# Kernel optimization log

Measured on AMD Instinct MI355X. Metric: run time of the kernel, lower is better.

Reference implementation:

```python
import jax, jax.numpy as jnp
import numpy as np

BN_EPS = 1e-5


def setup_inputs() -> dict:
    key = jax.random.key(0)
    ks = jax.random.split(key, 13)
    B, C, H, W = 8, 256, 96, 32
    D = C // 2  # inter_channels
    s = 0.05
    return {
        "x": jax.random.normal(ks[0], (B, C, H, W), jnp.float32),
        "g_w": jax.random.normal(ks[1], (D, C), jnp.float32) * s,
        "g_b": jax.random.normal(ks[2], (D,), jnp.float32) * s,
        "theta_w": jax.random.normal(ks[3], (D, C), jnp.float32) * s,
        "theta_b": jax.random.normal(ks[4], (D,), jnp.float32) * s,
        "phi_w": jax.random.normal(ks[5], (D, C), jnp.float32) * s,
        "phi_b": jax.random.normal(ks[6], (D,), jnp.float32) * s,
        "w_w": jax.random.normal(ks[7], (C, D), jnp.float32) * s,
        "w_b": jax.random.normal(ks[8], (C,), jnp.float32) * s,
        "bn_gamma": jax.random.normal(ks[9], (C,), jnp.float32),
        "bn_beta": jax.random.normal(ks[10], (C,), jnp.float32) * s,
        "bn_mean": jax.random.normal(ks[11], (C,), jnp.float32) * s,
        "bn_var": jax.random.uniform(ks[12], (C,), jnp.float32),
    }


def reference(x, g_w, g_b, theta_w, theta_b, phi_w, phi_b, w_w, w_b,
              bn_gamma, bn_beta, bn_mean, bn_var):
    B, C, H, W = x.shape
    N = H * W
    xf = x.reshape(B, C, N)  # flatten spatial: (B, C, N)

    # 1x1 conv projections == per-pixel linear maps
    g_x = jnp.einsum('dc,bcn->bnd', g_w, xf) + g_b            # (B, N, D)
    theta_x = jnp.einsum('dc,bcn->bnd', theta_w, xf) + theta_b  # (B, N, D)
    phi_x = jnp.einsum('dc,bcn->bdn', phi_w, xf) + phi_b[:, None]  # (B, D, N)

    # unnormalized attention: f = theta phi^T / N, then y = f g
    f_div_C = jnp.einsum('bnd,bdm->bnm', theta_x, phi_x) / N  # (B, N, N)
    y = jnp.einsum('bnm,bmd->bnd', f_div_C, g_x)              # (B, N, D)

    # output 1x1 conv + eval-mode BatchNorm2d
    wy = jnp.einsum('cd,bnd->bcn', w_w, y) + w_b[:, None]     # (B, C, N)
    inv = bn_gamma / jnp.sqrt(bn_var + BN_EPS)
    wy = (wy - bn_mean[:, None]) * inv[:, None] + bn_beta[:, None]

    z = wy.reshape(B, C, H, W) + x  # residual
    return z
```

## Files before the change

kernel.cpp:

```cpp
#include <hip/hip_runtime.h>
#include <hip/hip_bf16.h>
#include <cstddef>

typedef __attribute__((ext_vector_type(8))) short short8;
typedef __attribute__((ext_vector_type(4))) float floatx4;
typedef __hip_bfloat16 bf16;

#define NB 8
#define NC 256
#define ND 128
#define NN 3072
#define BN_EPS 1e-5f

static __device__ __forceinline__ short f2s(float v) {
    bf16 h = __float2bfloat16(v);
    return *reinterpret_cast<short*>(&h);
}

__global__ __launch_bounds__(384)
void proj_kernel(const float* __restrict__ x,
                 const float* __restrict__ phi_w, const float* __restrict__ g_w,
                 const float* __restrict__ theta_w,
                 const float* __restrict__ phi_b, const float* __restrict__ g_b,
                 const float* __restrict__ theta_b,
                 short* __restrict__ thND, float* __restrict__ Mbuf)
{
    __shared__ short Ws[384][72];
    __shared__ short Xs[64][72];
    int b = blockIdx.y;
    int n0 = blockIdx.x * 64;
    int t = threadIdx.x;
    int lane = t & 63;
    int wave = t >> 6;
    int lm = lane & 15;
    int lk = (lane >> 4) * 8;

    const float* xb = x + (size_t)b * NC * NN;

    int wk = (t & 7) * 8;
    int wr0 = t >> 3;

    floatx4 zero = {0.f, 0.f, 0.f, 0.f};
    floatx4 acc[4][4];
#pragma unroll
    for (int i = 0; i < 4; ++i)
#pragma unroll
        for (int j = 0; j < 4; ++j) acc[i][j] = zero;

#pragma unroll
    for (int kt = 0; kt < NC; kt += 64) {
        __syncthreads();
#pragma unroll
        for (int p = 0; p < 8; ++p) {
            int r = wr0 + p * 48;
            const float* src = (r < 128) ? (phi_w + (size_t)r * NC)
                             : (r < 256) ? (g_w + (size_t)(r - 128) * NC)
                                         : (theta_w + (size_t)(r - 256) * NC);
            src += kt + wk;
            floatx4 v0 = *(const floatx4*)src;
            floatx4 v1 = *(const floatx4*)(src + 4);
            short8 s;
#pragma unroll
            for (int j = 0; j < 4; ++j) { s[j] = f2s(v0[j]); s[4 + j] = f2s(v1[j]); }
            *(short8*)&Ws[r][wk] = s;
        }
        if (t < 256) {
            int sn = t & 63, cg = t >> 6;
            const float* src = xb + (size_t)(kt + cg * 16) * NN + n0 + sn;
            short8 s0, s1;
#pragma unroll
            for (int j = 0; j < 8; ++j) {
                s0[j] = f2s(src[(size_t)j * NN]);
                s1[j] = f2s(src[(size_t)(8 + j) * NN]);
            }
            *(short8*)&Xs[sn][cg * 16]     = s0;
            *(short8*)&Xs[sn][cg * 16 + 8] = s1;
        }
        __syncthreads();
#pragma unroll
        for (int kk = 0; kk < 64; kk += 32) {
            short8 af[4], bfr[4];
#pragma unroll
            for (int i = 0; i < 4; ++i)
                af[i] = *(const short8*)&Ws[wave * 64 + i * 16 + lm][kk + lk];
#pragma unroll
            for (int j = 0; j < 4; ++j)
                bfr[j] = *(const short8*)&Xs[j * 16 + lm][kk + lk];
#pragma unroll
            for (int i = 0; i < 4; ++i)
#pragma unroll
                for (int j = 0; j < 4; ++j)
                    acc[i][j] = __builtin_amdgcn_mfma_f32_16x16x32_bf16(
                        af[i], bfr[j], acc[i][j], 0, 0, 0);
        }
    }

    int row0 = wave * 64 + (lane >> 4) * 4;

    __syncthreads();
    if (wave < 4) {
#pragma unroll
        for (int i = 0; i < 4; ++i) {
#pragma unroll
            for (int r = 0; r < 4; ++r) {
                int row = row0 + i * 16 + r;
                float bv = (row < 128) ? phi_b[row] : g_b[row - 128];
#pragma unroll
                for (int j = 0; j < 4; ++j)
                    Ws[row][lm + j * 16] = f2s(acc[i][j][r] + bv);
            }
        }
    } else {
        short* Tb = thND + (size_t)b * NN * ND;
#pragma unroll
        for (int i = 0; i < 4; ++i) {
#pragma unroll
            for (int r = 0; r < 4; ++r) {
                int d = row0 - 256 + i * 16 + r;
                float bv = theta_b[d];
#pragma unroll
                for (int j = 0; j < 4; ++j)
                    Tb[(size_t)(n0 + lm + j * 16) * ND + d] =
                        f2s(acc[i][j][r] + bv);
            }
        }
    }
    __syncthreads();

    if (wave < 4) {
        int wr = wave >> 1, wc = wave & 1;
        floatx4 macc[4][4];
#pragma unroll
        for (int i = 0; i < 4; ++i)
#pragma unroll
            for (int j = 0; j < 4; ++j) macc[i][j] = zero;
#pragma unroll
        for (int kk = 0; kk < 64; kk += 32) {
            short8 af[4], bfr[4];
#pragma unroll
            for (int i = 0; i < 4; ++i)
                af[i] = *(const short8*)&Ws[wr * 64 + i * 16 + lm][kk + lk];
#pragma unroll
            for (int j = 0; j < 4; ++j)
                bfr[j] = *(const short8*)&Ws[128 + wc * 64 + j * 16 + lm][kk + lk];
#pragma unroll
            for (int i = 0; i < 4; ++i)
#pragma unroll
                for (int j = 0; j < 4; ++j)
                    macc[i][j] = __builtin_amdgcn_mfma_f32_16x16x32_bf16(
                        af[i], bfr[j], macc[i][j], 0, 0, 0);
        }
        float* Mf = Mbuf + (size_t)b * ND * ND;
        int mr0 = wr * 64 + (lane >> 4) * 4;
        int mc0 = wc * 64 + lm;
        const float sc = 1.f / (float)NN;
#pragma unroll
        for (int i = 0; i < 4; ++i)
#pragma unroll
            for (int j = 0; j < 4; ++j)
#pragma unroll
                for (int r = 0; r < 4; ++r)
                    atomicAdd(&Mf[(size_t)(mr0 + i * 16 + r) * ND + mc0 + j * 16],
                              macc[i][j][r] * sc);
    }
}

__global__ __launch_bounds__(256)
void final_kernel(const float* __restrict__ Mbuf, const short* __restrict__ thND,
                  const float* __restrict__ w_w, const float* __restrict__ w_b,
                  const float* __restrict__ gamma, const float* __restrict__ beta,
                  const float* __restrict__ mean, const float* __restrict__ var,
                  const float* __restrict__ x, float* __restrict__ out)
{
    __shared__ short As[128][72];
    __shared__ short Bs[128][72];
    __shared__ short P2s[128][132];
    int b = blockIdx.z;
    int tile_m = blockIdx.y * 128;
    int tile_n = blockIdx.x * 128;
    int t = threadIdx.x;
    int lane = t & 63;
    int wave = t >> 6;
    int wr = wave >> 1, wc = wave & 1;
    int lm = lane & 15;
    int lk = (lane >> 4) * 8;
    int ch = (t & 7) * 8;
    int r0 = t >> 3;

    const float* Mb = Mbuf + (size_t)b * ND * ND;

    floatx4 zero = {0.f, 0.f, 0.f, 0.f};
    floatx4 acc[4][4];
#pragma unroll
    for (int i = 0; i < 4; ++i)
#pragma unroll
        for (int j = 0; j < 4; ++j) acc[i][j] = zero;

#pragma unroll
    for (int kt = 0; kt < ND; kt += 64) {
        __syncthreads();
#pragma unroll
        for (int p = 0; p < 4; ++p) {
            int r = r0 + p * 32;
            const float* ap = w_w + (size_t)(tile_m + r) * ND + kt + ch;
            const float* bp = Mb + (size_t)r * ND + kt + ch;
            floatx4 a0 = *(const floatx4*)ap, a1 = *(const floatx4*)(ap + 4);
            floatx4 b0 = *(const floatx4*)bp, b1 = *(const floatx4*)(bp + 4);
            short8 sa, sb;
#pragma unroll
            for (int j = 0; j < 4; ++j) {
                sa[j] = f2s(a0[j]); sa[4 + j] = f2s(a1[j]);
                sb[j] = f2s(b0[j]); sb[4 + j] = f2s(b1[j]);
            }
            *(short8*)&As[r][ch] = sa;
            *(short8*)&Bs[r][ch] = sb;
        }
        __syncthreads();
#pragma unroll
        for (int kk = 0; kk < 64; kk += 32) {
            short8 af[4], bfr[4];
#pragma unroll
            for (int i = 0; i < 4; ++i)
                af[i] = *(const short8*)&As[wr * 64 + i * 16 + lm][kk + lk];
#pragma unroll
            for (int j = 0; j < 4; ++j)
                bfr[j] = *(const short8*)&Bs[wc * 64 + j * 16 + lm][kk + lk];
#pragma unroll
            for (int i = 0; i < 4; ++i)
#pragma unroll
                for (int j = 0; j < 4; ++j)
                    acc[i][j] = __builtin_amdgcn_mfma_f32_16x16x32_bf16(
                        af[i], bfr[j], acc[i][j], 0, 0, 0);
        }
    }

    {
        int row0 = wr * 64 + (lane >> 4) * 4;
        int col0 = wc * 64 + lm;
#pragma unroll
        for (int i = 0; i < 4; ++i) {
#pragma unroll
            for (int r = 0; r < 4; ++r) {
                int cl = row0 + i * 16 + r;
                int c = tile_m + cl;
                float iv = gamma[c] * rsqrtf(var[c] + BN_EPS);
#pragma unroll
                for (int j = 0; j < 4; ++j)
                    P2s[cl][col0 + j * 16] = f2s(acc[i][j][r] * iv);
            }
        }
    }
    __syncthreads();

    floatx4 acc2[4][4];
#pragma unroll
    for (int i = 0; i < 4; ++i)
#pragma unroll
        for (int j = 0; j < 4; ++j) acc2[i][j] = zero;

    const short* Tb = thND + (size_t)b * NN * ND;
#pragma unroll
    for (int kt = 0; kt < ND; kt += 64) {
        __syncthreads();
#pragma unroll
        for (int p = 0; p < 4; ++p) {
            int r = r0 + p * 32;
            *(short8*)&Bs[r][ch] =
                *(const short8*)(Tb + (size_t)(tile_n + r) * ND + kt + ch);
        }
        __syncthreads();
#pragma unroll
        for (int kk = 0; kk < 64; kk += 32) {
            short8 af[4], bfr[4];
#pragma unroll
            for (int i = 0; i < 4; ++i)
                af[i] = *(const short8*)&P2s[wr * 64 + i * 16 + lm][kt + kk + lk];
#pragma unroll
            for (int j = 0; j < 4; ++j)
                bfr[j] = *(const short8*)&Bs[wc * 64 + j * 16 + lm][kk + lk];
#pragma unroll
            for (int i = 0; i < 4; ++i)
#pragma unroll
                for (int j = 0; j < 4; ++j)
                    acc2[i][j] = __builtin_amdgcn_mfma_f32_16x16x32_bf16(
                        af[i], bfr[j], acc2[i][j], 0, 0, 0);
        }
    }

    int crow0 = tile_m + wr * 64 + (lane >> 4) * 4;
    int col0 = tile_n + wc * 64 + lm;
    float* Cf = out + (size_t)b * NC * NN;
    const float* Rg = x + (size_t)b * NC * NN;
#pragma unroll
    for (int i = 0; i < 4; ++i) {
#pragma unroll
        for (int r = 0; r < 4; ++r) {
            int c = crow0 + i * 16 + r;
            float iv = gamma[c] * rsqrtf(var[c] + BN_EPS);
            float b2 = iv * (w_b[c] - mean[c]) + beta[c];
#pragma unroll
            for (int j = 0; j < 4; ++j) {
                size_t idx = (size_t)c * NN + col0 + j * 16;
                Cf[idx] = acc2[i][j][r] + b2 + Rg[idx];
            }
        }
    }
}

extern "C" void kernel_launch(void* const* d_in, const int* in_sizes, int n_in,
                              void* d_out, int out_size, void* d_ws, size_t ws_size,
                              hipStream_t stream)
{
    const float* x       = (const float*)d_in[0];
    const float* g_w     = (const float*)d_in[1];
    const float* g_b     = (const float*)d_in[2];
    const float* theta_w = (const float*)d_in[3];
    const float* theta_b = (const float*)d_in[4];
    const float* phi_w   = (const float*)d_in[5];
    const float* phi_b   = (const float*)d_in[6];
    const float* w_w     = (const float*)d_in[7];
    const float* w_b     = (const float*)d_in[8];
    const float* gamma   = (const float*)d_in[9];
    const float* beta    = (const float*)d_in[10];
    const float* mean    = (const float*)d_in[11];
    const float* var     = (const float*)d_in[12];
    (void)in_sizes; (void)n_in; (void)out_size; (void)ws_size;

    char* w = (char*)d_ws;
    short* thND = (short*)w; w += (size_t)NB * NN * ND * 2;
    float* Mbuf = (float*)w; w += (size_t)NB * ND * ND * 4;

    proj_kernel<<<dim3(NN / 64, NB), dim3(384), 0, stream>>>(
        x, phi_w, g_w, theta_w, phi_b, g_b, theta_b, thND, Mbuf);

    final_kernel<<<dim3(NN / 128, NC / 128, NB), 256, 0, stream>>>(
        Mbuf, thND, w_w, w_b, gamma, beta, mean, var, x, (float*)d_out);
}
```

Measured before the change: 161.3 us.

## Pre-convert projection weights to bf16 and store theta transposed

Adds a small setup kernel that converts the phi/g/theta weights to bf16 once per call. The projection kernel then reads A-fragments directly from global memory instead of staging and converting them in shared memory per block. Theta output is stored in D-major layout so its writes are contiguous in N, and the final kernel transposes it into shared memory with scalar scatters. Two redundant barriers are removed. The costs are an extra launch, uncached-in-LDS global fragment loads, and possible LDS bank conflicts in the transpose.

```diff
diff --git a/kernel.cpp b/kernel.cpp
--- a/kernel.cpp
+++ b/kernel.cpp
@@ -17,15 +17,25 @@
     return *reinterpret_cast<short*>(&h);
 }
 
+__global__ __launch_bounds__(256) void setup_kernel(
+    const float* __restrict__ phi_w, const float* __restrict__ g_w,
+    const float* __restrict__ theta_w, short* __restrict__ Wall)
+{
+    int t = threadIdx.x;
+    int r = blockIdx.x;
+    const float* src = (r < 128) ? (phi_w + (size_t)r * NC)
+                     : (r < 256) ? (g_w + (size_t)(r - 128) * NC)
+                                 : (theta_w + (size_t)(r - 256) * NC);
+    Wall[(size_t)r * NC + t] = f2s(src[t]);
+}
+
 __global__ __launch_bounds__(384)
-void proj_kernel(const float* __restrict__ x,
-                 const float* __restrict__ phi_w, const float* __restrict__ g_w,
-                 const float* __restrict__ theta_w,
+void proj_kernel(const float* __restrict__ x, const short* __restrict__ Wall,
                  const float* __restrict__ phi_b, const float* __restrict__ g_b,
                  const float* __restrict__ theta_b,
-                 short* __restrict__ thND, float* __restrict__ Mbuf)
+                 short* __restrict__ thDN, float* __restrict__ Mbuf)
 {
-    __shared__ short Ws[384][72];
+    __shared__ short PGs[256][72];
     __shared__ short Xs[64][72];
     int b = blockIdx.y;
     int n0 = blockIdx.x * 64;
@@ -37,9 +47,6 @@
 
     const float* xb = x + (size_t)b * NC * NN;
 
-    int wk = (t & 7) * 8;
-    int wr0 = t >> 3;
-
     floatx4 zero = {0.f, 0.f, 0.f, 0.f};
     floatx4 acc[4][4];
 #pragma unroll
@@ -50,20 +57,6 @@
 #pragma unroll
     for (int kt = 0; kt < NC; kt += 64) {
         __syncthreads();
-#pragma unroll
-        for (int p = 0; p < 8; ++p) {
-            int r = wr0 + p * 48;
-            const float* src = (r < 128) ? (phi_w + (size_t)r * NC)
-                             : (r < 256) ? (g_w + (size_t)(r - 128) * NC)
-                                         : (theta_w + (size_t)(r - 256) * NC);
-            src += kt + wk;
-            floatx4 v0 = *(const floatx4*)src;
-            floatx4 v1 = *(const floatx4*)(src + 4);
-            short8 s;
-#pragma unroll
-            for (int j = 0; j < 4; ++j) { s[j] = f2s(v0[j]); s[4 + j] = f2s(v1[j]); }
-            *(short8*)&Ws[r][wk] = s;
-        }
         if (t < 256) {
             int sn = t & 63, cg = t >> 6;
             const float* src = xb + (size_t)(kt + cg * 16) * NN + n0 + sn;
@@ -82,7 +75,8 @@
             short8 af[4], bfr[4];
 #pragma unroll
             for (int i = 0; i < 4; ++i)
-                af[i] = *(const short8*)&Ws[wave * 64 + i * 16 + lm][kk + lk];
+                af[i] = *(const short8*)(Wall +
+                        (size_t)(wave * 64 + i * 16 + lm) * NC + kt + kk + lk);
 #pragma unroll
             for (int j = 0; j < 4; ++j)
                 bfr[j] = *(const short8*)&Xs[j * 16 + lm][kk + lk];
@@ -97,7 +91,6 @@
 
     int row0 = wave * 64 + (lane >> 4) * 4;
 
-    __syncthreads();
     if (wave < 4) {
 #pragma unroll
         for (int i = 0; i < 4; ++i) {
@@ -107,11 +100,11 @@
                 float bv = (row < 128) ? phi_b[row] : g_b[row - 128];
 #pragma unroll
                 for (int j = 0; j < 4; ++j)
-                    Ws[row][lm + j * 16] = f2s(acc[i][j][r] + bv);
+                    PGs[row][lm + j * 16] = f2s(acc[i][j][r] + bv);
             }
         }
     } else {
-        short* Tb = thND + (size_t)b * NN * ND;
+        short* Tb = thDN + (size_t)b * ND * NN;
 #pragma unroll
         for (int i = 0; i < 4; ++i) {
 #pragma unroll
@@ -120,7 +113,7 @@
                 float bv = theta_b[d];
 #pragma unroll
                 for (int j = 0; j < 4; ++j)
-                    Tb[(size_t)(n0 + lm + j * 16) * ND + d] =
+                    Tb[(size_t)d * NN + n0 + lm + j * 16] =
                         f2s(acc[i][j][r] + bv);
             }
         }
@@ -139,10 +132,10 @@
             short8 af[4], bfr[4];
 #pragma unroll
             for (int i = 0; i < 4; ++i)
-                af[i] = *(const short8*)&Ws[wr * 64 + i * 16 + lm][kk + lk];
-#pragma unroll
-            for (int j = 0; j < 4; ++j)
-                bfr[j] = *(const short8*)&Ws[128 + wc * 64 + j * 16 + lm][kk + lk];
+                af[i] = *(const short8*)&PGs[wr * 64 + i * 16 + lm][kk + lk];
+#pragma unroll
+            for (int j = 0; j < 4; ++j)
+                bfr[j] = *(const short8*)&PGs[128 + wc * 64 + j * 16 + lm][kk + lk];
 #pragma unroll
             for (int i = 0; i < 4; ++i)
 #pragma unroll
@@ -166,7 +159,7 @@
 }
 
 __global__ __launch_bounds__(256)
-void final_kernel(const float* __restrict__ Mbuf, const short* __restrict__ thND,
+void final_kernel(const float* __restrict__ Mbuf, const short* __restrict__ thDN,
                   const float* __restrict__ w_w, const float* __restrict__ w_b,
                   const float* __restrict__ gamma, const float* __restrict__ beta,
                   const float* __restrict__ mean, const float* __restrict__ var,
@@ -174,7 +167,7 @@
 {
     __shared__ short As[128][72];
     __shared__ short Bs[128][72];
-    __shared__ short P2s[128][132];
+    __shared__ short P2s[128][136];
     int b = blockIdx.z;
     int tile_m = blockIdx.y * 128;
     int tile_n = blockIdx.x * 128;
@@ -250,7 +243,6 @@
             }
         }
     }
-    __syncthreads();
 
     floatx4 acc2[4][4];
 #pragma unroll
@@ -258,15 +250,21 @@
 #pragma unroll
         for (int j = 0; j < 4; ++j) acc2[i][j] = zero;
 
-    const short* Tb = thND + (size_t)b * NN * ND;
+    const short* Tb = thDN + (size_t)b * ND * NN;
 #pragma unroll
     for (int kt = 0; kt < ND; kt += 64) {
         __syncthreads();
-#pragma unroll
-        for (int p = 0; p < 4; ++p) {
-            int r = r0 + p * 32;
-            *(short8*)&Bs[r][ch] =
-                *(const short8*)(Tb + (size_t)(tile_n + r) * ND + kt + ch);
+        {
+            int dl = t & 63;
+            int ng = t >> 6;
+            const short* src = Tb + (size_t)(kt + dl) * NN + tile_n + ng * 32;
+#pragma unroll
+            for (int q = 0; q < 4; ++q) {
+                short8 v = *(const short8*)(src + q * 8);
+#pragma unroll
+                for (int jj = 0; jj < 8; ++jj)
+                    Bs[ng * 32 + q * 8 + jj][dl] = v[jj];
+            }
         }
         __syncthreads();
 #pragma unroll
@@ -327,12 +325,16 @@
     (void)in_sizes; (void)n_in; (void)out_size; (void)ws_size;
 
     char* w = (char*)d_ws;
-    short* thND = (short*)w; w += (size_t)NB * NN * ND * 2;
+    short* thDN = (short*)w; w += (size_t)NB * ND * NN * 2;
     float* Mbuf = (float*)w; w += (size_t)NB * ND * ND * 4;
+    short* Wall = (short*)w; w += (size_t)384 * NC * 2;
+
+    setup_kernel<<<dim3(384), dim3(256), 0, stream>>>(
+        phi_w, g_w, theta_w, Wall);
 
     proj_kernel<<<dim3(NN / 64, NB), dim3(384), 0, stream>>>(
-        x, phi_w, g_w, theta_w, phi_b, g_b, theta_b, thND, Mbuf);
+        x, Wall, phi_b, g_b, theta_b, thDN, Mbuf);
 
     final_kernel<<<dim3(NN / 128, NC / 128, NB), 256, 0, stream>>>(
-        Mbuf, thND, w_w, w_b, gamma, beta, mean, var, x, (float*)d_out);
-}
+        Mbuf, thDN, w_w, w_b, gamma, beta, mean, var, x, (float*)d_out);
+}
```

Measured after the change: 160.0 us. No clear change (-0.8%).
